# Kernel optimization log

Measured on AMD Instinct MI355X. Metric: run time of the kernel, lower is better.

Reference implementation:

```python
import jax, jax.numpy as jnp
import numpy as np

N = 30000   # nodes
E = 480000  # edges
IN = 128    # hidden_dim (in_feats)
H = 4       # num_heads
D = 128     # out_feats per head
HD = H * D
NEG_SLOPE = 0.2
BN_EPS = 1e-5


def setup_inputs() -> dict:
    key = jax.random.key(0)
    ks = jax.random.split(key, 12)
    feat = jax.random.normal(ks[0], (N, IN), dtype=jnp.float32)
    src = jax.random.randint(ks[1], (E,), 0, N)
    dst = jax.random.randint(ks[2], (E,), 0, N)
    sc_in = 1.0 / np.sqrt(IN)
    sc_hd = 1.0 / np.sqrt(HD)
    W_fc = jax.random.normal(ks[3], (IN, HD), dtype=jnp.float32) * sc_in
    attn_l = jax.random.normal(ks[4], (H, D), dtype=jnp.float32) * sc_in
    attn_r = jax.random.normal(ks[5], (H, D), dtype=jnp.float32) * sc_in
    W_res = jax.random.normal(ks[6], (IN, HD), dtype=jnp.float32) * sc_in
    bias_gat = jnp.zeros((HD,), dtype=jnp.float32)
    gamma = jnp.ones((HD,), dtype=jnp.float32)
    beta = jnp.zeros((HD,), dtype=jnp.float32)
    W_out = jax.random.normal(ks[7], (HD, IN), dtype=jnp.float32) * sc_hd
    b_out = jnp.zeros((IN,), dtype=jnp.float32)
    return dict(feat=feat, src=src, dst=dst, W_fc=W_fc, attn_l=attn_l,
                attn_r=attn_r, W_res=W_res, bias_gat=bias_gat,
                gamma=gamma, beta=beta, W_out=W_out, b_out=b_out)


def reference(feat, src, dst, W_fc, attn_l, attn_r, W_res, bias_gat,
              gamma, beta, W_out, b_out):
    # --- GATConv (eval mode: dropout off) ---
    h = (feat @ W_fc).reshape(N, H, D)               # projected feats [N,H,D]
    el = jnp.einsum('nhd,hd->nh', h, attn_l)         # [N,H]
    er = jnp.einsum('nhd,hd->nh', h, attn_r)         # [N,H]
    e = el[src] + er[dst]                            # [E,H]
    e = jnp.where(e > 0, e, NEG_SLOPE * e)           # leaky_relu(0.2)
    # segment softmax over edges grouped by destination node
    emax = jax.ops.segment_max(e, dst, num_segments=N)   # [N,H]
    emax = jnp.where(jnp.isfinite(emax), emax, 0.0)      # empty segments
    ex = jnp.exp(e - emax[dst])                          # [E,H]
    denom = jax.ops.segment_sum(ex, dst, num_segments=N) # [N,H]
    a = ex / denom[dst]                                  # [E,H] attention
    msgs = h[src] * a[:, :, None]                        # [E,H,D]
    rst = jax.ops.segment_sum(msgs, dst, num_segments=N) # [N,H,D]
    # residual (in_feats != H*out_feats -> linear res_fc) + bias
    rst = rst + (feat @ W_res).reshape(N, H, D) + bias_gat.reshape(1, H, D)
    # --- fc_out: Flatten -> BatchNorm1d (train stats) -> ReLU -> Linear ---
    x = rst.reshape(N, HD)
    mu = x.mean(axis=0)
    var = x.var(axis=0)
    xn = (x - mu) / jnp.sqrt(var + BN_EPS)
    x = jnp.maximum(gamma * xn + beta, 0.0)
    return x @ W_out + b_out                             # [N, IN]
```

## Files before the change

### kernel.cpp

```cpp
#include <hip/hip_runtime.h>

#define N_  30000
#define E_  480000

typedef short short8 __attribute__((ext_vector_type(8)));
typedef float f32x4  __attribute__((ext_vector_type(4)));
typedef float f32x2  __attribute__((ext_vector_type(2)));
typedef unsigned int u32x4 __attribute__((ext_vector_type(4)));
typedef unsigned int u32x2 __attribute__((ext_vector_type(2)));
union Frag { u32x4 q; short8 v; unsigned short us[8]; };

__device__ __forceinline__ float b2f(unsigned short u){
  union { unsigned int i; float f; } v; v.i = ((unsigned int)u) << 16; return v.f;
}
__device__ __forceinline__ float blo(unsigned int u){
  union { unsigned int i; float f; } v; v.i = u << 16; return v.f;
}
__device__ __forceinline__ float bhi(unsigned int u){
  union { unsigned int i; float f; } v; v.i = u & 0xffff0000u; return v.f;
}
__device__ __forceinline__ unsigned short f2b(float f){
  union { float f; unsigned int u; } v; v.f = f;
  unsigned int u = v.u;
  return (unsigned short)((u + 0x7fffu + ((u >> 16) & 1u)) >> 16);
}

__global__ void k_initconv(const float* __restrict__ Wfc, const float* __restrict__ Wres,
                           const float* __restrict__ Wout,
                           unsigned short* __restrict__ Wt2, unsigned short* __restrict__ WtOut,
                           int* __restrict__ counts, int* __restrict__ cursor){
  int gid = blockIdx.x * 256 + threadIdx.x;
  int stride = gridDim.x * 256;
  if (gid < N_){ counts[gid] = 0; cursor[gid] = 0; }
  const int total1 = 512 * 256;
  const int total2 = 128 * 512;
  for (int i = gid; i < total1 + total2; i += stride){
    if (i < total1){
      int c = i >> 8, k = i & 255;
      float v = (k < 128) ? Wfc[k * 512 + c] : Wres[(k - 128) * 512 + c];
      Wt2[((k >> 7) << 16) + c * 128 + (k & 127)] = f2b(v);
    } else {
      int j = i - total1;
      int n = j >> 9, k = j & 511;
      WtOut[((k >> 7) << 14) + n * 128 + (k & 127)] = f2b(Wout[k * 128 + n]);
    }
  }
}

__global__ __launch_bounds__(128) void k_prep(const float* __restrict__ Wfc,
                                              const float* __restrict__ al,
                                              const float* __restrict__ ar,
                                              float* __restrict__ P){
  int idx = blockIdx.x * 128 + threadIdx.x;
  if (idx >= 1024) return;
  int k = idx >> 3, q = idx & 7;
  int h = q & 3;
  const float* a = (q < 4) ? al : ar;
  const float* wr = Wfc + k * 512 + h * 128;
  const float* av = a + h * 128;
  float s = 0.f;
#pragma unroll 4
  for (int d = 0; d < 128; d++) s += wr[d] * av[d];
  P[k * 8 + q] = s;
}

__global__ __launch_bounds__(256) void k_el(const float* __restrict__ feat,
                                            const float* __restrict__ P,
                                            float* __restrict__ el, float* __restrict__ er,
                                            unsigned short* __restrict__ featb){
  __shared__ float sF[32 * 132];
  __shared__ float sP[1024];
  int t = threadIdx.x;
  int n0 = blockIdx.x * 32;
  *reinterpret_cast<f32x4*>(&sP[t * 4]) = *reinterpret_cast<const f32x4*>(P + t * 4);
#pragma unroll
  for (int i = 0; i < 4; i++){
    int c = t + i * 256;
    int r = c >> 5, cw = (c & 31) * 4;
    int gn = n0 + r;
    f32x4 v = {0.f, 0.f, 0.f, 0.f};
    if (gn < N_) v = *reinterpret_cast<const f32x4*>(feat + gn * 128 + cw);
    *reinterpret_cast<f32x4*>(&sF[r * 132 + cw]) = v;
  }
  __syncthreads();
#pragma unroll
  for (int i = 0; i < 8; i++){
    int c = t + i * 256;
    int r = c >> 6, cw = (c & 63) * 2;
    int gn = n0 + r;
    if (gn < N_){
      float v0 = sF[r * 132 + cw], v1 = sF[r * 132 + cw + 1];
      unsigned int pv = (unsigned int)f2b(v0) | ((unsigned int)f2b(v1) << 16);
      *reinterpret_cast<unsigned int*>(featb + gn * 128 + cw) = pv;
    }
  }
  int node = t >> 3, q = t & 7;
  int gn = n0 + node;
  const float* fr = &sF[node * 132];
  float s = 0.f;
#pragma unroll 2
  for (int k = 0; k < 128; k += 4){
    f32x4 fv = *reinterpret_cast<const f32x4*>(fr + k);
#pragma unroll
    for (int j = 0; j < 4; j++) s += fv[j] * sP[(k + j) * 8 + q];
  }
  if (gn < N_){
    if (q < 4) el[gn * 4 + q] = s;
    else       er[gn * 4 + (q - 4)] = s;
  }
}

__global__ void k_hist(const int* __restrict__ dst, int* __restrict__ counts){
  int e = blockIdx.x * 256 + threadIdx.x;
  if (e < E_) atomicAdd(&counts[dst[e]], 1);
}

__global__ __launch_bounds__(1024) void k_scan(const int* __restrict__ counts,
                                               int* __restrict__ offs){
  __shared__ int wsum[16];
  int t = threadIdx.x;
  int lane = t & 63, w = t >> 6;
  int base = t * 32;
  int vals[32];
  int s = 0;
#pragma unroll
  for (int j = 0; j < 32; j++){
    int idx = base + j;
    int v = (idx < N_) ? counts[idx] : 0;
    vals[j] = s;
    s += v;
  }
  int x = s;
  for (int o = 1; o < 64; o <<= 1){
    int y = __shfl_up(x, o);
    if (lane >= o) x += y;
  }
  if (lane == 63) wsum[w] = x;
  __syncthreads();
  if (t < 16){
    int y = wsum[t];
    for (int o = 1; o < 16; o <<= 1){
      int z = __shfl_up(y, o, 16);
      if (t >= o) y += z;
    }
    wsum[t] = y;
  }
  __syncthreads();
  int wbase = (w > 0) ? wsum[w - 1] : 0;
  int ex = wbase + x - s;
#pragma unroll
  for (int j = 0; j < 32; j++){
    int idx = base + j;
    if (idx <= N_) offs[idx] = ex + vals[j];
  }
}

__global__ void k_edge(const int* __restrict__ src, const int* __restrict__ dst,
                       int* __restrict__ src_s,
                       const int* __restrict__ offs, int* __restrict__ cursor){
  int e = blockIdx.x * 256 + threadIdx.x;
  if (e >= E_) return;
  int d = dst[e];
  int p = atomicAdd(&cursor[d], 1);
  src_s[offs[d] + p] = src[e];
}

__global__ __launch_bounds__(256) void k_aggrf(const int* __restrict__ offs,
                                               const int* __restrict__ src_s,
                                               const float* __restrict__ el,
                                               const float* __restrict__ er,
                                               const unsigned short* __restrict__ featb,
                                               unsigned short* __restrict__ fagg){
  __shared__ float wls[4][512];
  int wave = threadIdx.x >> 6, lane = threadIdx.x & 63;
  int n = blockIdx.x * 4 + wave;
  if (n >= N_) return;
  int off0 = __builtin_amdgcn_readfirstlane(offs[n]);
  int g    = __builtin_amdgcn_readfirstlane(offs[n + 1]) - off0;
  int head = lane >> 4, sub = lane & 15;
  f32x4 er4 = *reinterpret_cast<const f32x4*>(er + n * 4);
  float ern = er4[head];

  float ssum = 0.f;
  for (int i = sub; i < g; i += 16){
    int s = src_s[off0 + i];
    float v = el[s * 4 + head] + ern;
    v = v > 0.f ? v : 0.2f * v;
    float w = __expf(v);
    if (i < 128) wls[wave][i * 4 + head] = w;
    ssum += w;
  }
#pragma unroll
  for (int o = 8; o >= 1; o >>= 1) ssum += __shfl_xor(ssum, o, 16);
  float rdh = (ssum > 0.f) ? 1.0f / ssum : 0.f;
  f32x4 rd4;
#pragma unroll
  for (int h = 0; h < 4; h++) rd4[h] = __shfl(rdh, h * 16 + sub);

  int c0 = lane * 2;
  f32x2 acc2[4] = {};
  auto FMA1 = [&](int ei, int s, unsigned int pv){
    f32x4 wv;
    if (ei < 128) wv = *reinterpret_cast<const f32x4*>(&wls[wave][ei * 4]);
    else {
      f32x4 evv = *reinterpret_cast<const f32x4*>(el + s * 4);
#pragma unroll
      for (int h = 0; h < 4; h++){
        float v = evv[h] + er4[h];
        v = v > 0.f ? v : 0.2f * v;
        wv[h] = __expf(v);
      }
    }
    f32x2 lh; lh[0] = blo(pv); lh[1] = bhi(pv);
#pragma unroll
    for (int h = 0; h < 4; h++) acc2[h] += lh * wv[h];
  };

  int i = 0;
  while (i < g){
    int blk = g - i; if (blk > 64) blk = 64;
    int idx = i + lane;
    int ssrc = (idx < g) ? src_s[off0 + idx] : 0;
    int nfull = blk >> 3;
    if (nfull){
      int sa[8]; unsigned int pa[8];
#pragma unroll
      for (int u = 0; u < 8; u++) sa[u] = __shfl(ssrc, u);
#pragma unroll
      for (int u = 0; u < 8; u++) pa[u] = *reinterpret_cast<const unsigned int*>(featb + sa[u] * 128 + c0);
      for (int c = 1; c < nfull; c++){
        int sb[8]; unsigned int pb[8];
#pragma unroll
        for (int u = 0; u < 8; u++) sb[u] = __shfl(ssrc, c * 8 + u);
#pragma unroll
        for (int u = 0; u < 8; u++) pb[u] = *reinterpret_cast<const unsigned int*>(featb + sb[u] * 128 + c0);
#pragma unroll
        for (int u = 0; u < 8; u++) FMA1(i + (c - 1) * 8 + u, sa[u], pa[u]);
#pragma unroll
        for (int u = 0; u < 8; u++){ sa[u] = sb[u]; pa[u] = pb[u]; }
      }
#pragma unroll
      for (int u = 0; u < 8; u++) FMA1(i + (nfull - 1) * 8 + u, sa[u], pa[u]);
    }
    for (int j = nfull * 8; j < blk; j++){
      int s = __shfl(ssrc, j);
      unsigned int pv = *reinterpret_cast<const unsigned int*>(featb + s * 128 + c0);
      FMA1(i + j, s, pv);
    }
    i += blk;
  }

#pragma unroll
  for (int h = 0; h < 4; h++){
    unsigned int ov = (unsigned int)f2b(acc2[h][0] * rd4[h]) |
                      ((unsigned int)f2b(acc2[h][1] * rd4[h]) << 16);
    *reinterpret_cast<unsigned int*>(fagg + n * 512 + h * 128 + c0) = ov;
  }
}

__global__ __launch_bounds__(512) void k_gemmC(const unsigned short* __restrict__ fagg,
                                               const unsigned short* __restrict__ featb,
                                               const unsigned short* __restrict__ Wt2,
                                               const float* __restrict__ bias,
                                               unsigned short* __restrict__ comb){
  __shared__ unsigned short wsl[256 * 128];
  char* wb = (char*)wsl;
  int tid = threadIdx.x;
  int wave = tid >> 6, lane = tid & 63;
  int lrow = lane & 15, quad = lane >> 4;
  int rowbase = blockIdx.x * 128 + wave * 16;
  int colbase = blockIdx.y * 256;
  int h0 = blockIdx.y * 2;
  int arow = rowbase + lrow; if (arow > N_ - 1) arow = N_ - 1;
  const unsigned short* aF = fagg + arow * 512 + h0 * 128;
  const unsigned short* aX = featb + arow * 128;
  f32x4 acc[16] = {};
  for (int phase = 0; phase < 2; phase++){
    __syncthreads();
#pragma unroll
    for (int i = 0; i < 8; i++){
      int c = tid + i * 512;
      int col = c >> 4, unit = c & 15;
      u32x4 v = *reinterpret_cast<const u32x4*>(Wt2 + (phase << 16) + (colbase + col) * 128 + unit * 8);
      int byte = (col * 256 + unit * 16) ^ ((col & 7) << 4);
      *reinterpret_cast<u32x4*>(wb + byte) = v;
    }
    __syncthreads();
#pragma unroll
    for (int kk = 0; kk < 4; kk++){
      Frag a0, a1;
      if (phase == 0){
        a0.q = *reinterpret_cast<const u32x4*>(aF + kk * 32 + quad * 8);
        a1.q = *reinterpret_cast<const u32x4*>(aF + 128 + kk * 32 + quad * 8);
      } else {
        a0.q = *reinterpret_cast<const u32x4*>(aX + kk * 32 + quad * 8);
        a1.q = a0.q;
      }
#pragma unroll
      for (int s = 0; s < 16; s++){
        int r = s * 16 + lrow;
        int byte = (r * 256 + kk * 64 + quad * 16) ^ ((r & 7) << 4);
        Frag b; b.q = *reinterpret_cast<const u32x4*>(wb + byte);
        acc[s] = __builtin_amdgcn_mfma_f32_16x16x32_bf16(b.v, (s < 8 ? a0.v : a1.v), acc[s], 0, 0, 0);
      }
    }
  }
  int gr = rowbase + lrow;
  if (gr < N_){
    unsigned short* crow = comb + gr * 512 + colbase;
#pragma unroll
    for (int s = 0; s < 16; s++){
      f32x4 bb = *reinterpret_cast<const f32x4*>(bias + colbase + s * 16 + quad * 4);
      u32x2 ov;
#pragma unroll
      for (int d = 0; d < 2; d++){
        float v0 = acc[s][2 * d]     + bb[2 * d];
        float v1 = acc[s][2 * d + 1] + bb[2 * d + 1];
        ov[d] = (unsigned int)f2b(v0) | ((unsigned int)f2b(v1) << 16);
      }
      *reinterpret_cast<u32x2*>(crow + s * 16 + quad * 4) = ov;
    }
  }
}

__global__ __launch_bounds__(256) void k_stats(const unsigned short* __restrict__ comb,
                                               float* __restrict__ psum,
                                               float* __restrict__ psq){
  __shared__ float lsum[4][512];
  __shared__ float lsq[4][512];
  int t = threadIdx.x, lane = t & 63, rg = t >> 6;
  int c0 = lane * 8;
  const int rows = 118;
  int r0 = blockIdx.x * rows;
  int r1 = r0 + rows; if (r1 > N_) r1 = N_;
  float s[8] = {}, q[8] = {};
  for (int r = r0 + rg; r < r1; r += 4){
    u32x4 pv = *reinterpret_cast<const u32x4*>(comb + r * 512 + c0);
#pragma unroll
    for (int d = 0; d < 4; d++){
      float v0 = blo(pv[d]);
      float v1 = bhi(pv[d]);
      s[2*d]   += v0; q[2*d]   += v0 * v0;
      s[2*d+1] += v1; q[2*d+1] += v1 * v1;
    }
  }
#pragma unroll
  for (int d = 0; d < 8; d++){ lsum[rg][c0 + d] = s[d]; lsq[rg][c0 + d] = q[d]; }
  __syncthreads();
#pragma unroll
  for (int half = 0; half < 2; half++){
    int ch = t + half * 256;
    float a = lsum[0][ch] + lsum[1][ch] + lsum[2][ch] + lsum[3][ch];
    float b = lsq[0][ch] + lsq[1][ch] + lsq[2][ch] + lsq[3][ch];
    psum[blockIdx.x * 512 + ch] = a;
    psq[blockIdx.x * 512 + ch] = b;
  }
}

__global__ __launch_bounds__(128) void k_bnfin(const float* __restrict__ psum,
                                               const float* __restrict__ psq,
                                               const float* __restrict__ gamma,
                                               const float* __restrict__ beta,
                                               float* __restrict__ scale,
                                               float* __restrict__ shift){
  int ch = blockIdx.x * 128 + threadIdx.x;
  float s0 = 0.f, s1 = 0.f, s2 = 0.f, s3 = 0.f;
  float q0 = 0.f, q1 = 0.f, q2 = 0.f, q3 = 0.f;
  for (int b = 0; b < 256; b += 4){
    s0 += psum[(b    ) * 512 + ch];
    s1 += psum[(b + 1) * 512 + ch];
    s2 += psum[(b + 2) * 512 + ch];
    s3 += psum[(b + 3) * 512 + ch];
    q0 += psq[(b    ) * 512 + ch];
    q1 += psq[(b + 1) * 512 + ch];
    q2 += psq[(b + 2) * 512 + ch];
    q3 += psq[(b + 3) * 512 + ch];
  }
  float sum = (s0 + s1) + (s2 + s3);
  float sq  = (q0 + q1) + (q2 + q3);
  float mu  = sum / (float)N_;
  float var = sq / (float)N_ - mu * mu;
  float inv = rsqrtf(var + 1e-5f);
  float sc  = gamma[ch] * inv;
  scale[ch] = sc;
  shift[ch] = beta[ch] - mu * sc;
}

__global__ __launch_bounds__(512) void k_gemm2(const unsigned short* __restrict__ comb,
                                               const unsigned short* __restrict__ WtOut,
                                               const float* __restrict__ scale,
                                               const float* __restrict__ shift,
                                               const float* __restrict__ bout,
                                               float* __restrict__ out){
  __shared__ float sc[512], sh[512];
  __shared__ unsigned short wsl[128 * 128];
  char* wb = (char*)wsl;
  int t = threadIdx.x;
  sc[t] = scale[t]; sh[t] = shift[t];
  int wave = t >> 6, lane = t & 63, lrow = lane & 15, quad = lane >> 4;
  int rowbase = blockIdx.x * 128 + wave * 16;
  int rr = rowbase + lrow; if (rr > N_ - 1) rr = N_ - 1;
  const unsigned short* arow = comb + rr * 512;
  f32x4 acc[8] = {};
  for (int phase = 0; phase < 4; phase++){
    __syncthreads();
#pragma unroll
    for (int i = 0; i < 4; i++){
      int c = t + i * 512;
      int col = c >> 4, unit = c & 15;
      u32x4 v = *reinterpret_cast<const u32x4*>(WtOut + (phase << 14) + col * 128 + unit * 8);
      int byte = (col * 256 + unit * 16) ^ ((col & 7) << 4);
      *reinterpret_cast<u32x4*>(wb + byte) = v;
    }
    __syncthreads();
#pragma unroll
    for (int kk = 0; kk < 4; kk++){
      int base = phase * 128 + kk * 32 + quad * 8;
      Frag a; a.q = *reinterpret_cast<const u32x4*>(arow + base);
#pragma unroll
      for (int i2 = 0; i2 < 8; i2++){
        float x = b2f(a.us[i2]);
        x = fmaf(x, sc[base + i2], sh[base + i2]);
        a.us[i2] = f2b(fmaxf(x, 0.0f));
      }
#pragma unroll
      for (int s = 0; s < 8; s++){
        int r = s * 16 + lrow;
        int byte = (r * 256 + kk * 64 + quad * 16) ^ ((r & 7) << 4);
        Frag b; b.q = *reinterpret_cast<const u32x4*>(wb + byte);
        acc[s] = __builtin_amdgcn_mfma_f32_16x16x32_bf16(b.v, a.v, acc[s], 0, 0, 0);
      }
    }
  }
  int gr = rowbase + lrow;
  if (gr < N_){
    float* orow = out + gr * 128;
#pragma unroll
    for (int s = 0; s < 8; s++){
      int cb = s * 16 + quad * 4;
      f32x4 bb = *reinterpret_cast<const f32x4*>(bout + cb);
      f32x4 ov;
#pragma unroll
      for (int j = 0; j < 4; j++) ov[j] = acc[s][j] + bb[j];
      *reinterpret_cast<f32x4*>(orow + cb) = ov;
    }
  }
}

extern "C" void kernel_launch(void* const* d_in, const int* in_sizes, int n_in,
                              void* d_out, int out_size, void* d_ws, size_t ws_size,
                              hipStream_t stream){
  const float* feat  = (const float*)d_in[0];
  const int*   src   = (const int*)d_in[1];
  const int*   dst   = (const int*)d_in[2];
  const float* Wfc   = (const float*)d_in[3];
  const float* al    = (const float*)d_in[4];
  const float* ar    = (const float*)d_in[5];
  const float* Wres  = (const float*)d_in[6];
  const float* bias  = (const float*)d_in[7];
  const float* gamma = (const float*)d_in[8];
  const float* beta  = (const float*)d_in[9];
  const float* Wout  = (const float*)d_in[10];
  const float* bout  = (const float*)d_in[11];
  float* out = (float*)d_out;

  char* ws = (char*)d_ws;
  unsigned short* comb  = (unsigned short*)(ws + 0);
  unsigned short* fagg  = (unsigned short*)(ws + 30720000);
  unsigned short* Wt2   = (unsigned short*)(ws + 61440000);
  unsigned short* WtOut = (unsigned short*)(ws + 61702144);
  float*          el    = (float*)(ws + 61833216);
  float*          er    = (float*)(ws + 62313216);
  int*            offs  = (int*)(ws + 70473216);
  int*            counts= (int*)(ws + 70593280);
  int*            cursor= (int*)(ws + 70713280);
  int*            src_s = (int*)(ws + 70833280);
  float*          psum  = (float*)(ws + 72753280);
  float*          psq   = (float*)(ws + 73277568);
  float*          scale = (float*)(ws + 73801856);
  float*          shift = (float*)(ws + 73803904);
  unsigned short* featb = (unsigned short*)(ws + 73805952);
  float*          P     = psum;

  k_initconv<<<256, 256, 0, stream>>>(Wfc, Wres, Wout, Wt2, WtOut, counts, cursor);
  k_prep<<<8, 128, 0, stream>>>(Wfc, al, ar, P);
  k_hist<<<(E_ + 255) / 256, 256, 0, stream>>>(dst, counts);
  k_scan<<<1, 1024, 0, stream>>>(counts, offs);
  k_el<<<(N_ + 31) / 32, 256, 0, stream>>>(feat, P, el, er, featb);
  k_edge<<<(E_ + 255) / 256, 256, 0, stream>>>(src, dst, src_s, offs, cursor);
  k_aggrf<<<(N_ + 3) / 4, 256, 0, stream>>>(offs, src_s, el, er, featb, fagg);
  dim3 gC((N_ + 127) / 128, 2);
  k_gemmC<<<gC, 512, 0, stream>>>(fagg, featb, Wt2, bias, comb);
  k_stats<<<256, 256, 0, stream>>>(comb, psum, psq);
  k_bnfin<<<4, 128, 0, stream>>>(psum, psq, gamma, beta, scale, shift);
  k_gemm2<<<(N_ + 127) / 128, 512, 0, stream>>>(comb, WtOut, scale, shift, bout, out);
}
```

Baseline: 276.7 us.

## Fuse BN stats into GEMM epilogue, precompute edge weights, merge prep kernel

k_prep is folded into k_initconv as extra blocks, and k_scan reads counts with vector loads. k_edge now computes the unnormalized exp attention weights per edge while scattering them in CSR order, so k_aggrf drops its separate softmax pass and accumulates the denominator inline. The BatchNorm sum and sum-of-squares move into the k_gemmC epilogue through shuffle and LDS reductions, which removes the k_stats kernel and its re-read of comb. In exchange k_edge does more work, and k_aggrf reads 16 bytes of weights per edge instead of recomputing them.

Measured after the change: 277.2 us. About the same (+0.2%).

```diff
diff --git a/kernel.cpp b/kernel.cpp
--- a/kernel.cpp
+++ b/kernel.cpp
@@ -8,6 +8,7 @@
 typedef float f32x2  __attribute__((ext_vector_type(2)));
 typedef unsigned int u32x4 __attribute__((ext_vector_type(4)));
 typedef unsigned int u32x2 __attribute__((ext_vector_type(2)));
+typedef int i32x4 __attribute__((ext_vector_type(4)));
 union Frag { u32x4 q; short8 v; unsigned short us[8]; };
 
 __device__ __forceinline__ float b2f(unsigned short u){
@@ -27,10 +28,28 @@
 
 __global__ void k_initconv(const float* __restrict__ Wfc, const float* __restrict__ Wres,
                            const float* __restrict__ Wout,
+                           const float* __restrict__ al, const float* __restrict__ ar,
                            unsigned short* __restrict__ Wt2, unsigned short* __restrict__ WtOut,
+                           float* __restrict__ P,
                            int* __restrict__ counts, int* __restrict__ cursor){
-  int gid = blockIdx.x * 256 + threadIdx.x;
-  int stride = gridDim.x * 256;
+  int bx = blockIdx.x;
+  if (bx >= 256){
+    int idx = (bx - 256) * 256 + threadIdx.x;
+    if (idx < 1024){
+      int k = idx >> 3, q = idx & 7;
+      int h = q & 3;
+      const float* a = (q < 4) ? al : ar;
+      const float* wr = Wfc + k * 512 + h * 128;
+      const float* av = a + h * 128;
+      float s = 0.f;
+#pragma unroll 4
+      for (int d = 0; d < 128; d++) s += wr[d] * av[d];
+      P[k * 8 + q] = s;
+    }
+    return;
+  }
+  int gid = bx * 256 + threadIdx.x;
+  const int stride = 256 * 256;
   if (gid < N_){ counts[gid] = 0; cursor[gid] = 0; }
   const int total1 = 512 * 256;
   const int total2 = 128 * 512;
@@ -47,23 +66,6 @@
   }
 }
 
-__global__ __launch_bounds__(128) void k_prep(const float* __restrict__ Wfc,
-                                              const float* __restrict__ al,
-                                              const float* __restrict__ ar,
-                                              float* __restrict__ P){
-  int idx = blockIdx.x * 128 + threadIdx.x;
-  if (idx >= 1024) return;
-  int k = idx >> 3, q = idx & 7;
-  int h = q & 3;
-  const float* a = (q < 4) ? al : ar;
-  const float* wr = Wfc + k * 512 + h * 128;
-  const float* av = a + h * 128;
-  float s = 0.f;
-#pragma unroll 4
-  for (int d = 0; d < 128; d++) s += wr[d] * av[d];
-  P[k * 8 + q] = s;
-}
-
 __global__ __launch_bounds__(256) void k_el(const float* __restrict__ feat,
                                             const float* __restrict__ P,
                                             float* __restrict__ el, float* __restrict__ er,
@@ -123,12 +125,18 @@
   int base = t * 32;
   int vals[32];
   int s = 0;
-#pragma unroll
-  for (int j = 0; j < 32; j++){
-    int idx = base + j;
-    int v = (idx < N_) ? counts[idx] : 0;
-    vals[j] = s;
-    s += v;
+  bool inb = (base < N_);
+#pragma unroll
+  for (int jj = 0; jj < 8; jj++){
+    i32x4 cv = {0, 0, 0, 0};
+    if (inb) cv = *reinterpret_cast<const i32x4*>(counts + base + jj * 4);
+#pragma unroll
+    for (int m = 0; m < 4; m++){
+      int idx = base + jj * 4 + m;
+      int v = (idx < N_) ? cv[m] : 0;
+      vals[jj * 4 + m] = s;
+      s += v;
+    }
   }
   int x = s;
   for (int o = 1; o < 64; o <<= 1){
@@ -156,61 +164,43 @@
 }
 
 __global__ void k_edge(const int* __restrict__ src, const int* __restrict__ dst,
-                       int* __restrict__ src_s,
+                       const float* __restrict__ el, const float* __restrict__ er,
+                       float* __restrict__ ws_s, int* __restrict__ src_s,
                        const int* __restrict__ offs, int* __restrict__ cursor){
   int e = blockIdx.x * 256 + threadIdx.x;
   if (e >= E_) return;
-  int d = dst[e];
+  int s = src[e], d = dst[e];
+  f32x4 a = *reinterpret_cast<const f32x4*>(el + s * 4);
+  f32x4 b = *reinterpret_cast<const f32x4*>(er + d * 4);
+  f32x4 v;
+#pragma unroll
+  for (int i = 0; i < 4; i++){
+    float x = a[i] + b[i];
+    x = x > 0.f ? x : 0.2f * x;
+    v[i] = __expf(x);
+  }
   int p = atomicAdd(&cursor[d], 1);
-  src_s[offs[d] + p] = src[e];
+  int pos = offs[d] + p;
+  *reinterpret_cast<f32x4*>(ws_s + pos * 4) = v;
+  src_s[pos] = s;
 }
 
 __global__ __launch_bounds__(256) void k_aggrf(const int* __restrict__ offs,
                                                const int* __restrict__ src_s,
-                                               const float* __restrict__ el,
-                                               const float* __restrict__ er,
+                                               const float* __restrict__ ws_s,
                                                const unsigned short* __restrict__ featb,
                                                unsigned short* __restrict__ fagg){
-  __shared__ float wls[4][512];
   int wave = threadIdx.x >> 6, lane = threadIdx.x & 63;
   int n = blockIdx.x * 4 + wave;
   if (n >= N_) return;
   int off0 = __builtin_amdgcn_readfirstlane(offs[n]);
   int g    = __builtin_amdgcn_readfirstlane(offs[n + 1]) - off0;
-  int head = lane >> 4, sub = lane & 15;
-  f32x4 er4 = *reinterpret_cast<const f32x4*>(er + n * 4);
-  float ern = er4[head];
-
-  float ssum = 0.f;
-  for (int i = sub; i < g; i += 16){
-    int s = src_s[off0 + i];
-    float v = el[s * 4 + head] + ern;
-    v = v > 0.f ? v : 0.2f * v;
-    float w = __expf(v);
-    if (i < 128) wls[wave][i * 4 + head] = w;
-    ssum += w;
-  }
-#pragma unroll
-  for (int o = 8; o >= 1; o >>= 1) ssum += __shfl_xor(ssum, o, 16);
-  float rdh = (ssum > 0.f) ? 1.0f / ssum : 0.f;
-  f32x4 rd4;
-#pragma unroll
-  for (int h = 0; h < 4; h++) rd4[h] = __shfl(rdh, h * 16 + sub);
-
   int c0 = lane * 2;
   f32x2 acc2[4] = {};
-  auto FMA1 = [&](int ei, int s, unsigned int pv){
-    f32x4 wv;
-    if (ei < 128) wv = *reinterpret_cast<const f32x4*>(&wls[wave][ei * 4]);
-    else {
-      f32x4 evv = *reinterpret_cast<const f32x4*>(el + s * 4);
-#pragma unroll
-      for (int h = 0; h < 4; h++){
-        float v = evv[h] + er4[h];
-        v = v > 0.f ? v : 0.2f * v;
-        wv[h] = __expf(v);
-      }
-    }
+  f32x4 wsum = {0.f, 0.f, 0.f, 0.f};
+
+  auto FMA1 = [&](const f32x4& wv, unsigned int pv){
+    wsum += wv;
     f32x2 lh; lh[0] = blo(pv); lh[1] = bhi(pv);
 #pragma unroll
     for (int h = 0; h < 4; h++) acc2[h] += lh * wv[h];
@@ -223,37 +213,45 @@
     int ssrc = (idx < g) ? src_s[off0 + idx] : 0;
     int nfull = blk >> 3;
     if (nfull){
-      int sa[8]; unsigned int pa[8];
+      int sa[8]; unsigned int pa[8]; f32x4 wa[8];
 #pragma unroll
       for (int u = 0; u < 8; u++) sa[u] = __shfl(ssrc, u);
 #pragma unroll
       for (int u = 0; u < 8; u++) pa[u] = *reinterpret_cast<const unsigned int*>(featb + sa[u] * 128 + c0);
+#pragma unroll
+      for (int u = 0; u < 8; u++) wa[u] = *reinterpret_cast<const f32x4*>(ws_s + (off0 + i + u) * 4);
       for (int c = 1; c < nfull; c++){
-        int sb[8]; unsigned int pb[8];
+        int sb[8]; unsigned int pb[8]; f32x4 wb[8];
 #pragma unroll
         for (int u = 0; u < 8; u++) sb[u] = __shfl(ssrc, c * 8 + u);
 #pragma unroll
         for (int u = 0; u < 8; u++) pb[u] = *reinterpret_cast<const unsigned int*>(featb + sb[u] * 128 + c0);
 #pragma unroll
-        for (int u = 0; u < 8; u++) FMA1(i + (c - 1) * 8 + u, sa[u], pa[u]);
-#pragma unroll
-        for (int u = 0; u < 8; u++){ sa[u] = sb[u]; pa[u] = pb[u]; }
-      }
-#pragma unroll
-      for (int u = 0; u < 8; u++) FMA1(i + (nfull - 1) * 8 + u, sa[u], pa[u]);
+        for (int u = 0; u < 8; u++) wb[u] = *reinterpret_cast<const f32x4*>(ws_s + (off0 + i + c * 8 + u) * 4);
+#pragma unroll
+        for (int u = 0; u < 8; u++) FMA1(wa[u], pa[u]);
+#pragma unroll
+        for (int u = 0; u < 8; u++){ pa[u] = pb[u]; wa[u] = wb[u]; }
+      }
+#pragma unroll
+      for (int u = 0; u < 8; u++) FMA1(wa[u], pa[u]);
     }
     for (int j = nfull * 8; j < blk; j++){
       int s = __shfl(ssrc, j);
       unsigned int pv = *reinterpret_cast<const unsigned int*>(featb + s * 128 + c0);
-      FMA1(i + j, s, pv);
+      f32x4 wv = *reinterpret_cast<const f32x4*>(ws_s + (off0 + i + j) * 4);
+      FMA1(wv, pv);
     }
     i += blk;
   }
 
+  f32x4 rd;
+#pragma unroll
+  for (int h = 0; h < 4; h++) rd[h] = (wsum[h] > 0.f) ? 1.0f / wsum[h] : 0.f;
 #pragma unroll
   for (int h = 0; h < 4; h++){
-    unsigned int ov = (unsigned int)f2b(acc2[h][0] * rd4[h]) |
-                      ((unsigned int)f2b(acc2[h][1] * rd4[h]) << 16);
+    unsigned int ov = (unsigned int)f2b(acc2[h][0] * rd[h]) |
+                      ((unsigned int)f2b(acc2[h][1] * rd[h]) << 16);
     *reinterpret_cast<unsigned int*>(fagg + n * 512 + h * 128 + c0) = ov;
   }
 }
@@ -262,7 +260,9 @@
                                                const unsigned short* __restrict__ featb,
                                                const unsigned short* __restrict__ Wt2,
                                                const float* __restrict__ bias,
-                                               unsigned short* __restrict__ comb){
+                                               unsigned short* __restrict__ comb,
+                                               float* __restrict__ psum,
+                                               float* __restrict__ psq){
   __shared__ unsigned short wsl[256 * 128];
   char* wb = (char*)wsl;
   int tid = threadIdx.x;
@@ -305,55 +305,53 @@
       }
     }
   }
+  __syncthreads();
+  float* psumL = (float*)wsl;
+  float* psqL  = (float*)wsl + 2048;
   int gr = rowbase + lrow;
-  if (gr < N_){
-    unsigned short* crow = comb + gr * 512 + colbase;
-#pragma unroll
-    for (int s = 0; s < 16; s++){
-      f32x4 bb = *reinterpret_cast<const f32x4*>(bias + colbase + s * 16 + quad * 4);
+  bool valid = (gr < N_);
+  unsigned short* crow = comb + gr * 512 + colbase;
+#pragma unroll
+  for (int s = 0; s < 16; s++){
+    f32x4 bb = *reinterpret_cast<const f32x4*>(bias + colbase + s * 16 + quad * 4);
+    f32x4 x, sv, qv;
+#pragma unroll
+    for (int j = 0; j < 4; j++){
+      x[j] = acc[s][j] + bb[j];
+      sv[j] = valid ? x[j] : 0.f;
+      qv[j] = sv[j] * x[j];
+    }
+    if (valid){
       u32x2 ov;
 #pragma unroll
-      for (int d = 0; d < 2; d++){
-        float v0 = acc[s][2 * d]     + bb[2 * d];
-        float v1 = acc[s][2 * d + 1] + bb[2 * d + 1];
-        ov[d] = (unsigned int)f2b(v0) | ((unsigned int)f2b(v1) << 16);
-      }
+      for (int d = 0; d < 2; d++)
+        ov[d] = (unsigned int)f2b(x[2*d]) | ((unsigned int)f2b(x[2*d+1]) << 16);
       *reinterpret_cast<u32x2*>(crow + s * 16 + quad * 4) = ov;
     }
-  }
-}
-
-__global__ __launch_bounds__(256) void k_stats(const unsigned short* __restrict__ comb,
-                                               float* __restrict__ psum,
-                                               float* __restrict__ psq){
-  __shared__ float lsum[4][512];
-  __shared__ float lsq[4][512];
-  int t = threadIdx.x, lane = t & 63, rg = t >> 6;
-  int c0 = lane * 8;
-  const int rows = 118;
-  int r0 = blockIdx.x * rows;
-  int r1 = r0 + rows; if (r1 > N_) r1 = N_;
-  float s[8] = {}, q[8] = {};
-  for (int r = r0 + rg; r < r1; r += 4){
-    u32x4 pv = *reinterpret_cast<const u32x4*>(comb + r * 512 + c0);
-#pragma unroll
-    for (int d = 0; d < 4; d++){
-      float v0 = blo(pv[d]);
-      float v1 = bhi(pv[d]);
-      s[2*d]   += v0; q[2*d]   += v0 * v0;
-      s[2*d+1] += v1; q[2*d+1] += v1 * v1;
-    }
-  }
-#pragma unroll
-  for (int d = 0; d < 8; d++){ lsum[rg][c0 + d] = s[d]; lsq[rg][c0 + d] = q[d]; }
+#pragma unroll
+    for (int o = 8; o >= 1; o >>= 1){
+#pragma unroll
+      for (int j = 0; j < 4; j++){
+        sv[j] += __shfl_xor(sv[j], o, 16);
+        qv[j] += __shfl_xor(qv[j], o, 16);
+      }
+    }
+    if (lrow == 0){
+      int ch = s * 16 + quad * 4;
+      *reinterpret_cast<f32x4*>(&psumL[wave * 256 + ch]) = sv;
+      *reinterpret_cast<f32x4*>(&psqL [wave * 256 + ch]) = qv;
+    }
+  }
   __syncthreads();
-#pragma unroll
-  for (int half = 0; half < 2; half++){
-    int ch = t + half * 256;
-    float a = lsum[0][ch] + lsum[1][ch] + lsum[2][ch] + lsum[3][ch];
-    float b = lsq[0][ch] + lsq[1][ch] + lsq[2][ch] + lsq[3][ch];
-    psum[blockIdx.x * 512 + ch] = a;
-    psq[blockIdx.x * 512 + ch] = b;
+  {
+    int ch = tid & 255;
+    const float* bufL = (tid < 256) ? psumL : psqL;
+    float a = 0.f;
+#pragma unroll
+    for (int w2 = 0; w2 < 8; w2++) a += bufL[w2 * 256 + ch];
+    float* gdst = (tid < 256) ? (psum + blockIdx.x * 512 + blockIdx.y * 256 + ch)
+                              : (psq  + blockIdx.x * 512 + blockIdx.y * 256 + ch);
+    *gdst = a;
   }
 }
 
@@ -364,20 +362,12 @@
                                                float* __restrict__ scale,
                                                float* __restrict__ shift){
   int ch = blockIdx.x * 128 + threadIdx.x;
-  float s0 = 0.f, s1 = 0.f, s2 = 0.f, s3 = 0.f;
-  float q0 = 0.f, q1 = 0.f, q2 = 0.f, q3 = 0.f;
-  for (int b = 0; b < 256; b += 4){
-    s0 += psum[(b    ) * 512 + ch];
-    s1 += psum[(b + 1) * 512 + ch];
-    s2 += psum[(b + 2) * 512 + ch];
-    s3 += psum[(b + 3) * 512 + ch];
-    q0 += psq[(b    ) * 512 + ch];
-    q1 += psq[(b + 1) * 512 + ch];
-    q2 += psq[(b + 2) * 512 + ch];
-    q3 += psq[(b + 3) * 512 + ch];
-  }
-  float sum = (s0 + s1) + (s2 + s3);
-  float sq  = (q0 + q1) + (q2 + q3);
+  float sum = 0.f, sq = 0.f;
+#pragma unroll 5
+  for (int b = 0; b < 235; b++){
+    sum += psum[b * 512 + ch];
+    sq  += psq [b * 512 + ch];
+  }
   float mu  = sum / (float)N_;
   float var = sq / (float)N_ - mu * mu;
   float inv = rsqrtf(var + 1e-5f);
@@ -471,6 +461,7 @@
   unsigned short* WtOut = (unsigned short*)(ws + 61702144);
   float*          el    = (float*)(ws + 61833216);
   float*          er    = (float*)(ws + 62313216);
+  float*          ws_s  = (float*)(ws + 62793216);
   int*            offs  = (int*)(ws + 70473216);
   int*            counts= (int*)(ws + 70593280);
   int*            cursor= (int*)(ws + 70713280);
@@ -482,16 +473,15 @@
   unsigned short* featb = (unsigned short*)(ws + 73805952);
   float*          P     = psum;
 
-  k_initconv<<<256, 256, 0, stream>>>(Wfc, Wres, Wout, Wt2, WtOut, counts, cursor);
-  k_prep<<<8, 128, 0, stream>>>(Wfc, al, ar, P);
+  k_initconv<<<260, 256, 0, stream>>>(Wfc, Wres, Wout, al, ar, Wt2, WtOut, P,
+                                      counts, cursor);
   k_hist<<<(E_ + 255) / 256, 256, 0, stream>>>(dst, counts);
   k_scan<<<1, 1024, 0, stream>>>(counts, offs);
   k_el<<<(N_ + 31) / 32, 256, 0, stream>>>(feat, P, el, er, featb);
-  k_edge<<<(E_ + 255) / 256, 256, 0, stream>>>(src, dst, src_s, offs, cursor);
-  k_aggrf<<<(N_ + 3) / 4, 256, 0, stream>>>(offs, src_s, el, er, featb, fagg);
+  k_edge<<<(E_ + 255) / 256, 256, 0, stream>>>(src, dst, el, er, ws_s, src_s, offs, cursor);
+  k_aggrf<<<(N_ + 3) / 4, 256, 0, stream>>>(offs, src_s, ws_s, featb, fagg);
   dim3 gC((N_ + 127) / 128, 2);
-  k_gemmC<<<gC, 512, 0, stream>>>(fagg, featb, Wt2, bias, comb);
-  k_stats<<<256, 256, 0, stream>>>(comb, psum, psq);
+  k_gemmC<<<gC, 512, 0, stream>>>(fagg, featb, Wt2, bias, comb, psum, psq);
   k_bnfin<<<4, 128, 0, stream>>>(psum, psq, gamma, beta, scale, shift);
   k_gemm2<<<(N_ + 127) / 128, 512, 0, stream>>>(comb, WtOut, scale, shift, bout, out);
 }
```
